# Kernel tuning notes

Hardware: AMD Instinct MI355X
Metric: run time of the kernel (lower is better)

## Reference

```python
import jax, jax.numpy as jnp
import numpy as np

B, H, W, D = 8, 56, 56, 256
NH = 8
KD = D // NH  # 32, key_dim == head_dim (value_factor=1)
FFN = 1024
EPS = 1e-6
SCALE = KD ** -0.5


def _lin(x, w, b):
    # torch nn.Linear: y = x @ W^T + b, W is (out, in)
    return jnp.einsum('...i,oi->...o', x, w) + b


def _ln(x, g, b):
    mu = jnp.mean(x, axis=-1, keepdims=True)
    var = jnp.mean(jnp.square(x - mu), axis=-1, keepdims=True)
    return (x - mu) * jax.lax.rsqrt(var + EPS) * g + b


def _dwconv(x, kernel, bias):
    # x: (B,H,W,C) NHWC, kernel: (kh,kw,1,C) HWIO depthwise
    y = jax.lax.conv_general_dilated(
        x, kernel, window_strides=(1, 1), padding='SAME',
        dimension_numbers=('NHWC', 'HWIO', 'NHWC'),
        feature_group_count=x.shape[-1])
    return y + bias


def _rope_sincos(h, w, head_dim):
    # PosEncodingGen: angle freq repeated pairwise, index over flattened H*W
    angle = 1.0 / (10000.0 ** jnp.linspace(0.0, 1.0, head_dim // 2))
    angle = jnp.repeat(angle, 2)  # (head_dim,)
    idx = jnp.arange(h * w, dtype=jnp.float32)
    phase = idx[:, None] * angle[None, :]
    return jnp.sin(phase).reshape(h, w, head_dim), jnp.cos(phase).reshape(h, w, head_dim)


def _angle_transform(x, sin, cos):
    # x: (B,NH,H,W,KD); sin/cos: (H,W,KD) broadcast over (B,NH)
    x1 = x[..., ::2]
    x2 = x[..., 1::2]
    rot = jnp.stack([-x2, x1], axis=-1).reshape(x.shape)
    return x * cos + rot * sin


def setup_inputs() -> dict:
    key = jax.random.key(0)
    ks = jax.random.split(key, 16)
    s = 0.02
    return {
        'x': jax.random.normal(ks[0], (B, H, W, D), jnp.float32),
        'cpe_w': jax.random.normal(ks[1], (3, 3, 1, D), jnp.float32) * s,
        'cpe_b': jnp.zeros((D,), jnp.float32),
        'ln1_g': jnp.ones((D,), jnp.float32),
        'ln1_b': jnp.zeros((D,), jnp.float32),
        'wq': jax.random.normal(ks[2], (D, D), jnp.float32) * s,
        'bq': jnp.zeros((D,), jnp.float32),
        'wk': jax.random.normal(ks[3], (D, D), jnp.float32) * s,
        'bk': jnp.zeros((D,), jnp.float32),
        'wv': jax.random.normal(ks[4], (D, D), jnp.float32) * s,
        'bv': jnp.zeros((D,), jnp.float32),
        'lepe_w': jax.random.normal(ks[5], (5, 5, 1, D), jnp.float32) * s,
        'lepe_b': jnp.zeros((D,), jnp.float32),
        'wo': jax.random.normal(ks[6], (D, D), jnp.float32) * s,
        'bo': jnp.zeros((D,), jnp.float32),
        'ln2_g': jnp.ones((D,), jnp.float32),
        'ln2_b': jnp.zeros((D,), jnp.float32),
        'fc1_w': jax.random.normal(ks[7], (FFN, D), jnp.float32) * s,
        'fc1_b': jnp.zeros((FFN,), jnp.float32),
        'dw_w': jax.random.normal(ks[8], (3, 3, 1, FFN), jnp.float32) * s,
        'dw_b': jnp.zeros((FFN,), jnp.float32),
        'fc2_w': jax.random.normal(ks[9], (D, FFN), jnp.float32) * s,
        'fc2_b': jnp.zeros((D,), jnp.float32),
    }


def _decomposed_gsa(x, sin, cos, wq, bq, wk, bk, wv, bv, lepe_w, lepe_b, wo, bo):
    b, h, w, d = x.shape
    q = _lin(x, wq, bq)
    k = _lin(x, wk, bk) * SCALE
    v = _lin(x, wv, bv)
    lepe = _dwconv(v, lepe_w, lepe_b)  # (b,h,w,d)
    # -> (b, nh, h, w, kd)
    q = q.reshape(b, h, w, NH, KD).transpose(0, 3, 1, 2, 4)
    k = k.reshape(b, h, w, NH, KD).transpose(0, 3, 1, 2, 4)
    v = v.reshape(b, h, w, NH, KD).transpose(0, 3, 1, 2, 4)
    qr = _angle_transform(q, sin, cos)
    kr = _angle_transform(k, sin, cos)
    # attention along W axis (per row h)
    aw = jnp.einsum('bnhik,bnhjk->bnhij', qr, kr)  # (b,nh,h,w,w)
    aw = jax.nn.softmax(aw, axis=-1)
    vw = jnp.einsum('bnhij,bnhjd->bnhid', aw, v)   # (b,nh,h,w,kd)
    # attention along H axis (per column w)
    ah = jnp.einsum('bniwk,bnjwk->bnwij', qr, kr)  # (b,nh,w,h,h)
    ah = jax.nn.softmax(ah, axis=-1)
    out = jnp.einsum('bnwij,bnjwd->bniwd', ah, vw)  # (b,nh,h,w,kd)
    # faithful to torch: flat reinterpret of (b,nh,h,w,kd) -> (b,h,w,nh*kd)
    out = out.reshape(b, h, w, NH * KD)
    out = out + lepe
    return _lin(out, wo, bo)


def reference(x, cpe_w, cpe_b, ln1_g, ln1_b, wq, bq, wk, bk, wv, bv,
              lepe_w, lepe_b, wo, bo, ln2_g, ln2_b,
              fc1_w, fc1_b, dw_w, dw_b, fc2_w, fc2_b):
    b, h, w, d = x.shape
    x = x + _dwconv(x, cpe_w, cpe_b)
    sin, cos = _rope_sincos(h, w, KD)
    # attention sub-block
    shortcut = x
    xn = _ln(x, ln1_g, ln1_b)
    attn = _decomposed_gsa(xn, sin, cos, wq, bq, wk, bk, wv, bv,
                           lepe_w, lepe_b, wo, bo)
    x = shortcut + attn  # drop_path=Identity, gamma_1=1.0
    # FFN sub-block (subconv=True, subln=False)
    shortcut = x
    xn = _ln(x, ln2_g, ln2_b)
    hdn = jax.nn.gelu(_lin(xn, fc1_w, fc1_b), approximate=False)
    hdn = _dwconv(hdn, dw_w, dw_b) + hdn
    ffn_out = _lin(hdn, fc2_w, fc2_b)
    return shortcut + ffn_out
```

## Files before the change

kernel.cpp:

```cpp
#include <hip/hip_runtime.h>
#include <hip/hip_bf16.h>
#include <math.h>

typedef __hip_bfloat16 bf16;

#define HB 8
#define HH 56
#define WWD 56
#define DD 256
#define NHEAD 8
#define KDIM 32
#define FFND 1024
#define NPIX (HB*HH*WWD)
#define SCALE_K 0.17677669529663687f

typedef __attribute__((ext_vector_type(8))) short short8;
typedef __attribute__((ext_vector_type(4))) float f32x4;

__device__ inline float toF(float x){ return x; }
__device__ inline float toF(bf16 x){ return __bfloat162float(x); }

__device__ inline float bfu_to_f(unsigned short u){
    union { float f; unsigned u32; } cv; cv.u32 = (unsigned)u << 16; return cv.f;
}

__device__ inline unsigned short f2bu(float f){
    union { bf16 b; unsigned short u; } cv; cv.b = __float2bfloat16(f); return cv.u;
}
__device__ inline unsigned pk2(float a, float b){
    return (unsigned)f2bu(a) | ((unsigned)f2bu(b) << 16);
}

__device__ inline void gl16(const bf16* g, unsigned short* l){
    __builtin_amdgcn_global_load_lds((const __attribute__((address_space(1))) void*)g,
                                     (__attribute__((address_space(3))) void*)l, 16, 0, 0);
}

__global__ __launch_bounds__(256) void wcvt_kernel(
    const float* __restrict__ wq, const float* __restrict__ wk,
    const float* __restrict__ wv, const float* __restrict__ wo,
    const float* __restrict__ f1, const float* __restrict__ f2,
    bf16* __restrict__ dst)
{
    const int id = blockIdx.x*256 + threadIdx.x;
    const float* src; int off;
    if      (id < 8192)  { src = wq; off = id; }
    else if (id < 16384) { src = wk; off = id - 8192; }
    else if (id < 24576) { src = wv; off = id - 16384; }
    else if (id < 32768) { src = wo; off = id - 24576; }
    else if (id < 65536) { src = f1; off = id - 32768; }
    else                 { src = f2; off = id - 65536; }
    const float4 a = *(const float4*)(src + (size_t)off*8);
    const float4 b = *(const float4*)(src + (size_t)off*8 + 4);
    uint4 v; v.x = pk2(a.x,a.y); v.y = pk2(a.z,a.w); v.z = pk2(b.x,b.y); v.w = pk2(b.z,b.w);
    *(uint4*)(dst + (size_t)id*8) = v;
}

__global__ __launch_bounds__(256) void rope_init_kernel(float2* __restrict__ t)
{
    const int id = blockIdx.x*256 + threadIdx.x;
    const int idx = id >> 4, i = id & 15;
    const float ph = (float)idx * exp2f(-(float)i * 0.88584749196996324f);
    t[id] = make_float2(cosf(ph), sinf(ph));
}

__global__ __launch_bounds__(256) void cpe_ln_kernel(
    const float* __restrict__ x, const float* __restrict__ wt,
    const float* __restrict__ bias, const float* __restrict__ g,
    const float* __restrict__ bln, float* __restrict__ X0, bf16* __restrict__ B1)
{
    constexpr int C = 256, VEC = 4, CG = 64, PPB = 4, KS = 3, P = 1;
    const int tid = threadIdx.x;
    const int cg  = tid % CG;
    const int pl  = tid / CG;
    const int p   = blockIdx.x * PPB + pl;
    const int w   = p % WWD;
    const int h   = (p / WWD) % HH;
    const int b   = p / (WWD * HH);
    const int c0  = cg * VEC;

    float acc[VEC];
    {
        const float4 b0 = *(const float4*)(bias + c0);
        acc[0] = b0.x; acc[1] = b0.y; acc[2] = b0.z; acc[3] = b0.w;
    }
    #pragma unroll
    for (int ky = 0; ky < KS; ky++) {
        const int hh = h + ky - P;
        if (hh < 0 || hh >= HH) continue;
        #pragma unroll
        for (int kx = 0; kx < KS; kx++) {
            const int ww = w + kx - P;
            if (ww < 0 || ww >= WWD) continue;
            const float4 wv = *(const float4*)(wt + (size_t)(ky*KS + kx)*C + c0);
            const float4 f0 = *(const float4*)(x + ((size_t)((b*HH + hh)*WWD + ww))*C + c0);
            acc[0] += f0.x * wv.x; acc[1] += f0.y * wv.y;
            acc[2] += f0.z * wv.z; acc[3] += f0.w * wv.w;
        }
    }
    const size_t obase = (size_t)p*C + c0;
    {
        const float4 f0 = *(const float4*)(x + obase);
        acc[0] += f0.x; acc[1] += f0.y; acc[2] += f0.z; acc[3] += f0.w;
    }
    { float4 o; o.x = acc[0]; o.y = acc[1]; o.z = acc[2]; o.w = acc[3];
      *(float4*)(X0 + obase) = o; }
    float s1 = acc[0] + acc[1] + acc[2] + acc[3];
    float s2 = acc[0]*acc[0] + acc[1]*acc[1] + acc[2]*acc[2] + acc[3]*acc[3];
    #pragma unroll
    for (int d = 1; d < 64; d <<= 1) { s1 += __shfl_xor(s1, d); s2 += __shfl_xor(s2, d); }
    const float mu  = s1 * (1.0f/DD);
    const float var = s2 * (1.0f/DD) - mu*mu;
    const float inv = rsqrtf(var + 1e-6f);
    const float4 gv = *(const float4*)(g + c0);
    const float4 bv = *(const float4*)(bln + c0);
    uint2 o;
    o.x = pk2((acc[0]-mu)*inv*gv.x + bv.x, (acc[1]-mu)*inv*gv.y + bv.y);
    o.y = pk2((acc[2]-mu)*inv*gv.z + bv.z, (acc[3]-mu)*inv*gv.w + bv.w);
    *(uint2*)(B1 + obase) = o;
}

template<int KS, bool ADD, int C>
__global__ __launch_bounds__(256) void dwconv_slide_kernel(
    const bf16* __restrict__ in, const float* __restrict__ wt, int wst,
    const float* __restrict__ bias, bf16* __restrict__ out)
{
    constexpr int VEC = 8, CG = C/VEC, GPB = 256/CG, NPX = 4, P = KS/2, NX = NPX+KS-1;
    constexpr int GPR = WWD/NPX;
    constexpr int NB  = NPIX/(NPX*GPB);
    const int tid = threadIdx.x;
    const int cg  = tid % CG;
    const int gl  = tid / CG;
    const int bid = blockIdx.x;
    const int swb = (bid & 7) * (NB >> 3) + (bid >> 3);
    const int gid = swb * GPB + gl;
    const int row = gid / GPR;
    const int w0  = (gid % GPR) * NPX;
    const int h   = row % HH;
    const int b   = row / HH;
    const int c0  = cg * VEC;

    float acc[NPX][VEC];
    {
        const float4 b0 = *(const float4*)(bias + c0);
        const float4 b1 = *(const float4*)(bias + c0 + 4);
        #pragma unroll
        for (int j = 0; j < NPX; j++) {
            acc[j][0]=b0.x; acc[j][1]=b0.y; acc[j][2]=b0.z; acc[j][3]=b0.w;
            acc[j][4]=b1.x; acc[j][5]=b1.y; acc[j][6]=b1.z; acc[j][7]=b1.w;
        }
    }

    #pragma unroll
    for (int ky = 0; ky < KS; ky++) {
        const int hh = h + ky - P;
        if (hh < 0 || hh >= HH) continue;
        const bf16* rowp = in + ((size_t)(b*HH + hh) * WWD) * C + c0;
        float wv[KS][VEC];
        #pragma unroll
        for (int kx = 0; kx < KS; kx++) {
            const float* wp = wt + (size_t)(ky*KS + kx)*wst + c0;
            const float4 w0v = *(const float4*)(wp);
            const float4 w1v = *(const float4*)(wp + 4);
            wv[kx][0]=w0v.x; wv[kx][1]=w0v.y; wv[kx][2]=w0v.z; wv[kx][3]=w0v.w;
            wv[kx][4]=w1v.x; wv[kx][5]=w1v.y; wv[kx][6]=w1v.z; wv[kx][7]=w1v.w;
        }
        #pragma unroll
        for (int x = 0; x < NX; x++) {
            const int ww = w0 - P + x;
            short8 raw = {0,0,0,0,0,0,0,0};
            if (ww >= 0 && ww < WWD) raw = *(const short8*)(rowp + (size_t)ww*C);
            float f[VEC];
            #pragma unroll
            for (int e = 0; e < VEC; e++) f[e] = bfu_to_f((unsigned short)raw[e]);
            #pragma unroll
            for (int j = 0; j < NPX; j++) {
                const int kx = x - j;
                if (kx < 0 || kx >= KS) continue;
                #pragma unroll
                for (int e = 0; e < VEC; e++)
                    acc[j][e] += f[e] * wv[kx][e];
            }
        }
    }

    #pragma unroll
    for (int j = 0; j < NPX; j++) {
        const size_t obase = ((size_t)row*WWD + w0 + j)*C + c0;
        if constexpr (ADD) {
            short8 vv = *(const short8*)(in + obase);
            #pragma unroll
            for (int e = 0; e < VEC; e++) acc[j][e] += bfu_to_f((unsigned short)vv[e]);
        }
        uint4 o;
        o.x = pk2(acc[j][0], acc[j][1]); o.y = pk2(acc[j][2], acc[j][3]);
        o.z = pk2(acc[j][4], acc[j][5]); o.w = pk2(acc[j][6], acc[j][7]);
        *(uint4*)(out + obase) = o;
    }
}

__global__ __launch_bounds__(256) void ln_kernel(
    const float* __restrict__ x, const float* __restrict__ g,
    const float* __restrict__ b, bf16* __restrict__ out)
{
    const int wv   = threadIdx.x >> 6;
    const int lane = threadIdx.x & 63;
    const int t    = blockIdx.x * 4 + wv;
    const float4 xv = *(const float4*)(x + (size_t)t*DD + lane*4);
    float s1 = xv.x + xv.y + xv.z + xv.w;
    float s2 = xv.x*xv.x + xv.y*xv.y + xv.z*xv.z + xv.w*xv.w;
    #pragma unroll
    for (int d = 1; d < 64; d <<= 1) {
        s1 += __shfl_xor(s1, d);
        s2 += __shfl_xor(s2, d);
    }
    const float mu  = s1 * (1.0f/DD);
    const float var = s2 * (1.0f/DD) - mu*mu;
    const float inv = rsqrtf(var + 1e-6f);
    const float4 gv = *(const float4*)(g + lane*4);
    const float4 bv = *(const float4*)(b + lane*4);
    uint2 o;
    o.x = pk2((xv.x-mu)*inv*gv.x + bv.x, (xv.y-mu)*inv*gv.y + bv.y);
    o.y = pk2((xv.z-mu)*inv*gv.z + bv.z, (xv.w-mu)*inv*gv.w + bv.w);
    *(uint2*)(out + (size_t)t*DD + lane*4) = o;
}

template<int EPI, int ROPE>
__global__ __launch_bounds__(256) void mgemm128_kernel(
    const bf16* __restrict__ A, const bf16* __restrict__ Wb, int ldw,
    const float* __restrict__ bias, const float2* __restrict__ ropet,
    const float* __restrict__ residF, float* __restrict__ accF,
    bf16* __restrict__ outB, bf16* __restrict__ outK, bf16* __restrict__ outV,
    int M, int N, int K, float scale)
{
    __shared__ __align__(16) unsigned short Sh[16384];
    const int tid  = threadIdx.x;
    const int wid  = tid >> 6;
    const int lane = tid & 63;
    const int quad = lane >> 4;
    const int l15  = lane & 15;
    const int wr   = wid >> 1;
    const int wc   = wid & 1;

    const int NXg = gridDim.x;
    const int T   = NXg * gridDim.y;
    int f = blockIdx.y * NXg + blockIdx.x;
    f = (f & 7) * (T >> 3) + (f >> 3);
    const int row0 = (f / NXg) * 128;
    const int col0 = (f % NXg) * 128;

    f32x4 acc[4][4];
    #pragma unroll
    for (int m = 0; m < 4; m++)
        #pragma unroll
        for (int n = 0; n < 4; n++)
            acc[m][n] = (f32x4){0.f, 0.f, 0.f, 0.f};

    const int ob0 = (wid*2 + 0)*64;
    const int ob1 = (wid*2 + 1)*64;
    const int o0  = ob0 + lane, o1 = ob1 + lane;
    const int rA0 = o0 >> 2, ch0 = (o0 & 3)*8;
    const int rA1 = o1 >> 2, ch1 = (o1 & 3)*8;
    const bf16* pA0 = A  + (size_t)(row0 + rA0)*K   + ch0;
    const bf16* pA1 = A  + (size_t)(row0 + rA1)*K   + ch1;
    const bf16* pW0 = Wb + (size_t)(col0 + rA0)*ldw + ch0;
    const bf16* pW1 = Wb + (size_t)(col0 + rA1)*ldw + ch1;

    #define STAGE(bi) { unsigned short* As_ = Sh + (bi)*8192;                  \
                        unsigned short* Bs_ = Sh + (bi)*8192 + 4096;           \
                        gl16(pA0, &As_[ob0*8]); gl16(pA1, &As_[ob1*8]);        \
                        gl16(pW0, &Bs_[ob0*8]); gl16(pW1, &Bs_[ob1*8]);        \
                        pA0 += 32; pA1 += 32; pW0 += 32; pW1 += 32; }

    #define COMPUTE(bi) { const unsigned short* As_ = Sh + (bi)*8192;          \
                          const unsigned short* Bs_ = Sh + (bi)*8192 + 4096;   \
                          short8 af[4], bfr[4];                                \
                          _Pragma("unroll")                                    \
                          for (int m = 0; m < 4; m++)                          \
                              af[m] = *(const short8*)(&As_[(wr*64 + m*16 + l15)*32 + quad*8]); \
                          _Pragma("unroll")                                    \
                          for (int n = 0; n < 4; n++)                          \
                              bfr[n] = *(const short8*)(&Bs_[(wc*64 + n*16 + l15)*32 + quad*8]); \
                          _Pragma("unroll")                                    \
                          for (int m = 0; m < 4; m++)                          \
                              _Pragma("unroll")                                \
                              for (int n = 0; n < 4; n++)                      \
                                  acc[m][n] = __builtin_amdgcn_mfma_f32_16x16x32_bf16(af[m], bfr[n], acc[m][n], 0, 0, 0); }

    const int nt = K >> 5;
    STAGE(0);
    int cur = 0;
    for (int t = 0; t < nt - 1; t++) {
        STAGE(cur ^ 1);
        asm volatile("s_waitcnt vmcnt(4)" ::: "memory");
        __builtin_amdgcn_s_barrier();
        COMPUTE(cur);
        __builtin_amdgcn_s_barrier();
        cur ^= 1;
    }
    asm volatile("s_waitcnt vmcnt(0)" ::: "memory");
    __builtin_amdgcn_s_barrier();
    COMPUTE(cur);
    #undef STAGE
    #undef COMPUTE

    __syncthreads();
    float* Ls = (float*)Sh;
    const int cbl = l15 * 4;
    const int seg = (EPI == 3) ? (col0 >> 8) : 0;
    bf16* dst = outB;
    if (EPI == 3) dst = (seg == 0) ? outB : ((seg == 1) ? outK : outV);
    const float esc = (EPI == 3) ? ((seg == 1) ? scale : 1.0f) : scale;
    const bool doRope = ROPE && (EPI != 3 || seg < 2);

    #pragma unroll
    for (int m = 0; m < 4; m++) {
        #pragma unroll
        for (int n = 0; n < 4; n++) {
            const int col = n*16 + l15;
            const float bval = bias[col0 + wc*64 + col];
            #pragma unroll
            for (int reg = 0; reg < 4; reg++) {
                float y = (acc[m][n][reg] + bval) * esc;
                if (EPI == 1) y = 0.5f*y*(1.0f + erff(y*0.70710678118654752f));
                Ls[wid*1088 + (quad*4+reg)*68 + col] = y;
            }
        }
        #pragma unroll
        for (int p = 0; p < 4; p++) {
            const int rowt = p*4 + quad;
            const float4 v = *(const float4*)&Ls[wid*1088 + rowt*68 + cbl];
            const int mm = row0 + wr*64 + m*16 + rowt;
            if (EPI == 2) {
                const size_t o = (size_t)mm * N + col0 + wc*64 + cbl;
                const float4 rv = *(const float4*)(residF + o);
                float4 w; w.x = v.x+rv.x; w.y = v.y+rv.y; w.z = v.z+rv.z; w.w = v.w+rv.w;
                *(float4*)(accF + o) = w;
            } else {
                const int ncl = (EPI == 3) ? ((col0 & 255) + wc*64 + cbl)
                                           : (col0 + wc*64 + cbl);
                const size_t o = (EPI == 3) ? ((size_t)mm * 256 + ncl)
                                            : ((size_t)mm * N + ncl);
                float a = v.x, b = v.y, c = v.z, d = v.w;
                if (doRope) {
                    const int idx = mm % (HH*WWD);
                    const int i0 = (ncl & 31) >> 1;
                    const float4 t = *(const float4*)&ropet[(size_t)idx*16 + i0];
                    const float na  = a*t.x - b*t.y;
                    const float nb  = b*t.x + a*t.y;
                    const float ncv = c*t.z - d*t.w;
                    const float nd  = d*t.z + c*t.w;
                    a = na; b = nb; c = ncv; d = nd;
                }
                uint2 ov; ov.x = pk2(a, b); ov.y = pk2(c, d);
                *(uint2*)(dst + o) = ov;
            }
        }
        if (m < 3) __syncthreads();
    }
}

template<bool COLM>
__global__ __launch_bounds__(256) void attn_mfma_kernel(
    const bf16* __restrict__ q, const bf16* __restrict__ k,
    const bf16* __restrict__ v, const bf16* __restrict__ lepe,
    bf16* __restrict__ outp)
{
    __shared__ unsigned short Qb[64*40];
    __shared__ unsigned short Kb[64*40];
    __shared__ unsigned short Vt[32*80];
    __shared__ unsigned short Pb[64*72];

    const int bid  = blockIdx.x;
    const int line = bid % 56;
    const int nh   = (bid / 56) % NHEAD;
    const int b    = bid / (56 * NHEAD);
    const int tid  = threadIdx.x;
    const int wid  = tid >> 6;
    const int lane = tid & 63;
    const int quad = lane >> 4;
    const int l15  = lane & 15;

    const size_t rstr = COLM ? (size_t)WWD * DD : (size_t)DD;
    const size_t base = COLM ? (((size_t)b*HH*WWD + line) * DD + nh*KDIM)
                             : (((size_t)(b*HH + line) * WWD) * DD + nh*KDIM);

    {
        const int r  = tid >> 2;
        const int cc = tid & 3;
        uint4 zero = {0,0,0,0};
        if (r < 56) {
            size_t g = base + (size_t)r * rstr + cc*8;
            *(uint4*)(&Qb[r*40 + cc*8]) = *(const uint4*)(q + g);
            *(uint4*)(&Kb[r*40 + cc*8]) = *(const uint4*)(k + g);
        } else {
            *(uint4*)(&Qb[r*40 + cc*8]) = zero;
            *(uint4*)(&Kb[r*40 + cc*8]) = zero;
        }
        uint4 vv = zero;
        if (lane < 56)
            vv = *(const uint4*)(v + base + (size_t)lane * rstr + wid*8);
        const unsigned short* pv = (const unsigned short*)&vv;
        #pragma unroll
        for (int e = 0; e < 8; e++)
            Vt[(wid*8 + e)*80 + lane] = pv[e];
    }
    __syncthreads();

    {
        short8 af = *(const short8*)(&Qb[(wid*16 + l15)*40 + quad*8]);
        f32x4 s_[4];
        #pragma unroll
        for (int j = 0; j < 4; j++) {
            short8 bfm = *(const short8*)(&Kb[(j*16 + l15)*40 + quad*8]);
            f32x4 z = {0.f,0.f,0.f,0.f};
            s_[j] = __builtin_amdgcn_mfma_f32_16x16x32_bf16(af, bfm, z, 0, 0, 0);
        }
        const bool v3 = (l15 < 8);
        float mx[4], sm[4];
        #pragma unroll
        for (int reg = 0; reg < 4; reg++) {
            float m01 = fmaxf(s_[0][reg], s_[1][reg]);
            float m23 = v3 ? fmaxf(s_[2][reg], s_[3][reg]) : s_[2][reg];
            mx[reg] = fmaxf(m01, m23);
        }
        #pragma unroll
        for (int d = 1; d < 16; d <<= 1) {
            #pragma unroll
            for (int reg = 0; reg < 4; reg++)
                mx[reg] = fmaxf(mx[reg], __shfl_xor(mx[reg], d));
        }
        float e_[4][4];
        #pragma unroll
        for (int reg = 0; reg < 4; reg++) sm[reg] = 0.f;
        #pragma unroll
        for (int j = 0; j < 4; j++) {
            #pragma unroll
            for (int reg = 0; reg < 4; reg++) {
                const bool valid = (j < 3) || v3;
                float ex = valid ? expf(s_[j][reg] - mx[reg]) : 0.f;
                e_[j][reg] = ex;
                sm[reg] += ex;
            }
        }
        #pragma unroll
        for (int d = 1; d < 16; d <<= 1) {
            #pragma unroll
            for (int reg = 0; reg < 4; reg++)
                sm[reg] += __shfl_xor(sm[reg], d);
        }
        float inv[4];
        #pragma unroll
        for (int reg = 0; reg < 4; reg++) inv[reg] = 1.0f / sm[reg];
        #pragma unroll
        for (int j = 0; j < 4; j++)
            #pragma unroll
            for (int reg = 0; reg < 4; reg++)
                Pb[(wid*16 + quad*4 + reg)*72 + j*16 + l15] = f2bu(e_[j][reg] * inv[reg]);
    }
    __syncthreads();

    {
        f32x4 acc[2];
        acc[0] = (f32x4){0.f,0.f,0.f,0.f};
        acc[1] = (f32x4){0.f,0.f,0.f,0.f};
        #pragma unroll
        for (int k0 = 0; k0 < 64; k0 += 32) {
            short8 af = *(const short8*)(&Pb[(wid*16 + l15)*72 + k0 + quad*8]);
            #pragma unroll
            for (int nt = 0; nt < 2; nt++) {
                short8 bfm = *(const short8*)(&Vt[(nt*16 + l15)*80 + k0 + quad*8]);
                acc[nt] = __builtin_amdgcn_mfma_f32_16x16x32_bf16(af, bfm, acc[nt], 0, 0, 0);
            }
        }
        #pragma unroll
        for (int nt = 0; nt < 2; nt++) {
            #pragma unroll
            for (int reg = 0; reg < 4; reg++) {
                const int m = wid*16 + quad*4 + reg;
                const int d = nt*16 + l15;
                if (m < 56) {
                    float val = acc[nt][reg];
                    if (COLM) {
                        int hp = 7*nh + (m >> 3);
                        int wp = (m & 7)*7 + (line >> 3);
                        int cp = (line & 7)*32 + d;
                        size_t o = ((size_t)(b*HH + hp)*WWD + wp)*DD + cp;
                        outp[o] = __float2bfloat16(val + toF(lepe[o]));
                    } else {
                        outp[base + (size_t)m * rstr + d] = __float2bfloat16(val);
                    }
                }
            }
        }
    }
}

extern "C" void kernel_launch(void* const* d_in, const int* in_sizes, int n_in,
                              void* d_out, int out_size, void* d_ws, size_t ws_size,
                              hipStream_t stream)
{
    const float* x_in   = (const float*)d_in[0];
    const float* cpe_w  = (const float*)d_in[1];
    const float* cpe_b  = (const float*)d_in[2];
    const float* ln1_g  = (const float*)d_in[3];
    const float* ln1_b  = (const float*)d_in[4];
    const float* wq     = (const float*)d_in[5];
    const float* bq     = (const float*)d_in[6];
    const float* wk     = (const float*)d_in[7];
    const float* bk     = (const float*)d_in[8];
    const float* wv     = (const float*)d_in[9];
    const float* bv     = (const float*)d_in[10];
    const float* lepe_w = (const float*)d_in[11];
    const float* lepe_b = (const float*)d_in[12];
    const float* wo     = (const float*)d_in[13];
    const float* bo     = (const float*)d_in[14];
    const float* ln2_g  = (const float*)d_in[15];
    const float* ln2_b  = (const float*)d_in[16];
    const float* fc1_w  = (const float*)d_in[17];
    const float* fc1_b  = (const float*)d_in[18];
    const float* dw_w   = (const float*)d_in[19];
    const float* dw_b   = (const float*)d_in[20];
    const float* fc2_w  = (const float*)d_in[21];
    const float* fc2_b  = (const float*)d_in[22];
    float* out = (float*)d_out;

    const size_t ND = (size_t)NPIX * DD;
    const size_t NF = (size_t)NPIX * FFND;
    char* ws = (char*)d_ws;
    float*  X0    = (float*)(ws);
    float*  ACC   = (float*)(ws + ND*4);
    bf16*   B1    = (bf16*) (ws + ND*8);
    bf16*   B2    = (bf16*) (ws + ND*8 + ND*2);
    bf16*   H1    = (bf16*) (ws + ND*8 + ND*4);
    bf16*   H2    = (bf16*) (ws + ND*8 + ND*4 + NF*2);
    bf16*   WB    = (bf16*) (ws + ND*8 + ND*4 + NF*4);
    float2* ROPET = (float2*)(ws + ND*8 + ND*4 + NF*4 + 786432*2);
    float*  BQKV  = (float*) (ws + ND*8 + ND*4 + NF*4 + 786432*2 + 50176*8);
    bf16*   B3 = H1;
    bf16*   B4 = H2;
    bf16*   VWb   = (bf16*)d_out;
    bf16*   ATTNb = VWb + ND;

    const bf16* WOb = WB + 196608;
    const bf16* F1b = WB + 262144;
    const bf16* F2b = WB + 524288;

    dim3 b256(256);
    dim3 gridQKV(768/128, NPIX/128);
    dim3 gridD(DD/128, NPIX/128);
    dim3 gridF(FFND/128, NPIX/128);

    wcvt_kernel<<<384, b256, 0, stream>>>(wq, wk, wv, wo, fc1_w, fc2_w, WB);
    rope_init_kernel<<<196, b256, 0, stream>>>(ROPET);
    hipMemcpyAsync(BQKV,       bq, 256*sizeof(float), hipMemcpyDeviceToDevice, stream);
    hipMemcpyAsync(BQKV + 256, bk, 256*sizeof(float), hipMemcpyDeviceToDevice, stream);
    hipMemcpyAsync(BQKV + 512, bv, 256*sizeof(float), hipMemcpyDeviceToDevice, stream);
    cpe_ln_kernel<<<NPIX/4, b256, 0, stream>>>(x_in, cpe_w, cpe_b, ln1_g, ln1_b, X0, B1);
    mgemm128_kernel<3,1><<<gridQKV, b256, 0, stream>>>(B1, WB, DD, BQKV, ROPET,
                                                       nullptr, nullptr, B2, B3, B4,
                                                       NPIX, 768, DD, SCALE_K);
    dwconv_slide_kernel<5, false, 256><<<784, b256, 0, stream>>>(B4, lepe_w, DD, lepe_b, B1);
    attn_mfma_kernel<false><<<HB*NHEAD*HH, b256, 0, stream>>>(B2, B3, B4, nullptr, VWb);
    attn_mfma_kernel<true><<<HB*NHEAD*WWD, b256, 0, stream>>>(B2, B3, VWb, B1, ATTNb);
    mgemm128_kernel<2,0><<<gridD, b256, 0, stream>>>(ATTNb, WOb, DD, bo, nullptr,
                                                     X0, ACC, nullptr, nullptr, nullptr,
                                                     NPIX, DD, DD, 1.0f);
    ln_kernel<<<NPIX/4, b256, 0, stream>>>(ACC, ln2_g, ln2_b, B2);
    mgemm128_kernel<1,0><<<gridF, b256, 0, stream>>>(B2, F1b, DD, fc1_b, nullptr,
                                                     nullptr, nullptr, H1, nullptr, nullptr,
                                                     NPIX, FFND, DD, 1.0f);
    dwconv_slide_kernel<3, true, 1024><<<3136, b256, 0, stream>>>(H1, dw_w, FFND, dw_b, H2);
    mgemm128_kernel<2,0><<<gridD, b256, 0, stream>>>(H2, F2b, FFND, fc2_b, nullptr,
                                                     ACC, out, nullptr, nullptr, nullptr,
                                                     NPIX, DD, FFND, 1.0f);
}
```

Baseline: 330.5 us.

## Triple-buffer GEMM K-loop and use sliding-window CPE+LayerNorm kernel

The bf16 MFMA GEMM moves from a double-buffered to a triple-buffered LDS pipeline, keeping two K-tiles of global loads in flight and adjusting waitcnt thresholds. The goal is to hide more global-load latency. In exchange, LDS per block grows to 48KB, which lowers occupancy. Separately, the CPE depthwise conv + LayerNorm kernel now has each wave compute 4 adjacent pixels. This reuses loaded input columns and weights across horizontal taps and cuts redundant global reads.

```diff
diff --git a/kernel.cpp b/kernel.cpp
--- a/kernel.cpp
+++ b/kernel.cpp
@@ -64,60 +64,87 @@
     t[id] = make_float2(cosf(ph), sinf(ph));
 }
 
-__global__ __launch_bounds__(256) void cpe_ln_kernel(
+__global__ __launch_bounds__(256) void cpe_ln_slide_kernel(
     const float* __restrict__ x, const float* __restrict__ wt,
     const float* __restrict__ bias, const float* __restrict__ g,
     const float* __restrict__ bln, float* __restrict__ X0, bf16* __restrict__ B1)
 {
-    constexpr int C = 256, VEC = 4, CG = 64, PPB = 4, KS = 3, P = 1;
-    const int tid = threadIdx.x;
-    const int cg  = tid % CG;
-    const int pl  = tid / CG;
-    const int p   = blockIdx.x * PPB + pl;
-    const int w   = p % WWD;
-    const int h   = (p / WWD) % HH;
-    const int b   = p / (WWD * HH);
-    const int c0  = cg * VEC;
-
-    float acc[VEC];
+    constexpr int C = 256, VEC = 4, NPX = 4, KS = 3, P = 1, NX = NPX + KS - 1;
+    constexpr int GPR = WWD / NPX;
+    constexpr int NB  = NPIX / (NPX * 4);
+    const int tid  = threadIdx.x;
+    const int wv   = tid >> 6;
+    const int lane = tid & 63;
+    const int bid  = blockIdx.x;
+    const int swb  = (bid & 7) * (NB >> 3) + (bid >> 3);
+    const int gid  = swb * 4 + wv;
+    const int row  = gid / GPR;
+    const int w0   = (gid % GPR) * NPX;
+    const int h    = row % HH;
+    const int b    = row / HH;
+    const int c0   = lane * VEC;
+
+    float acc[NPX][VEC];
     {
         const float4 b0 = *(const float4*)(bias + c0);
-        acc[0] = b0.x; acc[1] = b0.y; acc[2] = b0.z; acc[3] = b0.w;
-    }
+        #pragma unroll
+        for (int j = 0; j < NPX; j++) {
+            acc[j][0] = b0.x; acc[j][1] = b0.y; acc[j][2] = b0.z; acc[j][3] = b0.w;
+        }
+    }
+
     #pragma unroll
     for (int ky = 0; ky < KS; ky++) {
         const int hh = h + ky - P;
         if (hh < 0 || hh >= HH) continue;
+        const float* rowp = x + ((size_t)(b*HH + hh) * WWD) * C + c0;
+        float wvv[KS][VEC];
         #pragma unroll
         for (int kx = 0; kx < KS; kx++) {
-            const int ww = w + kx - P;
-            if (ww < 0 || ww >= WWD) continue;
-            const float4 wv = *(const float4*)(wt + (size_t)(ky*KS + kx)*C + c0);
-            const float4 f0 = *(const float4*)(x + ((size_t)((b*HH + hh)*WWD + ww))*C + c0);
-            acc[0] += f0.x * wv.x; acc[1] += f0.y * wv.y;
-            acc[2] += f0.z * wv.z; acc[3] += f0.w * wv.w;
-        }
-    }
-    const size_t obase = (size_t)p*C + c0;
-    {
-        const float4 f0 = *(const float4*)(x + obase);
-        acc[0] += f0.x; acc[1] += f0.y; acc[2] += f0.z; acc[3] += f0.w;
-    }
-    { float4 o; o.x = acc[0]; o.y = acc[1]; o.z = acc[2]; o.w = acc[3];
-      *(float4*)(X0 + obase) = o; }
-    float s1 = acc[0] + acc[1] + acc[2] + acc[3];
-    float s2 = acc[0]*acc[0] + acc[1]*acc[1] + acc[2]*acc[2] + acc[3]*acc[3];
-    #pragma unroll
-    for (int d = 1; d < 64; d <<= 1) { s1 += __shfl_xor(s1, d); s2 += __shfl_xor(s2, d); }
-    const float mu  = s1 * (1.0f/DD);
-    const float var = s2 * (1.0f/DD) - mu*mu;
-    const float inv = rsqrtf(var + 1e-6f);
+            const float4 w4 = *(const float4*)(wt + (size_t)(ky*KS + kx)*C + c0);
+            wvv[kx][0] = w4.x; wvv[kx][1] = w4.y; wvv[kx][2] = w4.z; wvv[kx][3] = w4.w;
+        }
+        #pragma unroll
+        for (int xc = 0; xc < NX; xc++) {
+            const int ww = w0 - P + xc;
+            float4 f0 = {0.f, 0.f, 0.f, 0.f};
+            if (ww >= 0 && ww < WWD) f0 = *(const float4*)(rowp + (size_t)ww*C);
+            const float fv[VEC] = {f0.x, f0.y, f0.z, f0.w};
+            #pragma unroll
+            for (int j = 0; j < NPX; j++) {
+                const int kx = xc - j;
+                if (kx < 0 || kx >= KS) continue;
+                #pragma unroll
+                for (int e = 0; e < VEC; e++)
+                    acc[j][e] += fv[e] * wvv[kx][e];
+            }
+        }
+    }
+
     const float4 gv = *(const float4*)(g + c0);
     const float4 bv = *(const float4*)(bln + c0);
-    uint2 o;
-    o.x = pk2((acc[0]-mu)*inv*gv.x + bv.x, (acc[1]-mu)*inv*gv.y + bv.y);
-    o.y = pk2((acc[2]-mu)*inv*gv.z + bv.z, (acc[3]-mu)*inv*gv.w + bv.w);
-    *(uint2*)(B1 + obase) = o;
+    #pragma unroll
+    for (int j = 0; j < NPX; j++) {
+        const size_t obase = ((size_t)row*WWD + w0 + j)*C + c0;
+        {
+            const float4 r0 = *(const float4*)(x + obase);
+            acc[j][0] += r0.x; acc[j][1] += r0.y; acc[j][2] += r0.z; acc[j][3] += r0.w;
+        }
+        { float4 o; o.x = acc[j][0]; o.y = acc[j][1]; o.z = acc[j][2]; o.w = acc[j][3];
+          *(float4*)(X0 + obase) = o; }
+        float s1 = acc[j][0] + acc[j][1] + acc[j][2] + acc[j][3];
+        float s2 = acc[j][0]*acc[j][0] + acc[j][1]*acc[j][1]
+                 + acc[j][2]*acc[j][2] + acc[j][3]*acc[j][3];
+        #pragma unroll
+        for (int d = 1; d < 64; d <<= 1) { s1 += __shfl_xor(s1, d); s2 += __shfl_xor(s2, d); }
+        const float mu  = s1 * (1.0f/DD);
+        const float var = s2 * (1.0f/DD) - mu*mu;
+        const float inv = rsqrtf(var + 1e-6f);
+        uint2 o2;
+        o2.x = pk2((acc[j][0]-mu)*inv*gv.x + bv.x, (acc[j][1]-mu)*inv*gv.y + bv.y);
+        o2.y = pk2((acc[j][2]-mu)*inv*gv.z + bv.z, (acc[j][3]-mu)*inv*gv.w + bv.w);
+        *(uint2*)(B1 + obase) = o2;
+    }
 }
 
 template<int KS, bool ADD, int C>
@@ -233,7 +260,7 @@
     bf16* __restrict__ outB, bf16* __restrict__ outK, bf16* __restrict__ outV,
     int M, int N, int K, float scale)
 {
-    __shared__ __align__(16) unsigned short Sh[16384];
+    __shared__ __align__(16) unsigned short Sh[24576];
     const int tid  = threadIdx.x;
     const int wid  = tid >> 6;
     const int lane = tid & 63;
@@ -267,13 +294,13 @@
     const bf16* pW1 = Wb + (size_t)(col0 + rA1)*ldw + ch1;
 
     #define STAGE(bi) { unsigned short* As_ = Sh + (bi)*8192;                  \
-                        unsigned short* Bs_ = Sh + (bi)*8192 + 4096;           \
+                        unsigned short* Bs_ = As_ + 4096;                      \
                         gl16(pA0, &As_[ob0*8]); gl16(pA1, &As_[ob1*8]);        \
                         gl16(pW0, &Bs_[ob0*8]); gl16(pW1, &Bs_[ob1*8]);        \
                         pA0 += 32; pA1 += 32; pW0 += 32; pW1 += 32; }
 
     #define COMPUTE(bi) { const unsigned short* As_ = Sh + (bi)*8192;          \
-                          const unsigned short* Bs_ = Sh + (bi)*8192 + 4096;   \
+                          const unsigned short* Bs_ = As_ + 4096;              \
                           short8 af[4], bfr[4];                                \
                           _Pragma("unroll")                                    \
                           for (int m = 0; m < 4; m++)                          \
@@ -288,19 +315,23 @@
                                   acc[m][n] = __builtin_amdgcn_mfma_f32_16x16x32_bf16(af[m], bfr[n], acc[m][n], 0, 0, 0); }
 
     const int nt = K >> 5;
-    STAGE(0);
+    STAGE(0); STAGE(1);
     int cur = 0;
-    for (int t = 0; t < nt - 1; t++) {
-        STAGE(cur ^ 1);
-        asm volatile("s_waitcnt vmcnt(4)" ::: "memory");
+    for (int t = 0; t < nt; t++) {
+        if (t + 2 < nt) {
+            const int nx = (cur == 0) ? 2 : ((cur == 1) ? 0 : 1);
+            STAGE(nx);
+            asm volatile("s_waitcnt vmcnt(8)" ::: "memory");
+        } else if (t + 1 < nt) {
+            asm volatile("s_waitcnt vmcnt(4)" ::: "memory");
+        } else {
+            asm volatile("s_waitcnt vmcnt(0)" ::: "memory");
+        }
         __builtin_amdgcn_s_barrier();
         COMPUTE(cur);
-        __builtin_amdgcn_s_barrier();
-        cur ^= 1;
-    }
-    asm volatile("s_waitcnt vmcnt(0)" ::: "memory");
-    __builtin_amdgcn_s_barrier();
-    COMPUTE(cur);
+        if (t + 1 < nt) __builtin_amdgcn_s_barrier();
+        cur = (cur == 2) ? 0 : cur + 1;
+    }
     #undef STAGE
     #undef COMPUTE
 
@@ -556,7 +587,7 @@
     hipMemcpyAsync(BQKV,       bq, 256*sizeof(float), hipMemcpyDeviceToDevice, stream);
     hipMemcpyAsync(BQKV + 256, bk, 256*sizeof(float), hipMemcpyDeviceToDevice, stream);
     hipMemcpyAsync(BQKV + 512, bv, 256*sizeof(float), hipMemcpyDeviceToDevice, stream);
-    cpe_ln_kernel<<<NPIX/4, b256, 0, stream>>>(x_in, cpe_w, cpe_b, ln1_g, ln1_b, X0, B1);
+    cpe_ln_slide_kernel<<<NPIX/16, b256, 0, stream>>>(x_in, cpe_w, cpe_b, ln1_g, ln1_b, X0, B1);
     mgemm128_kernel<3,1><<<gridQKV, b256, 0, stream>>>(B1, WB, DD, BQKV, ROPET,
                                                        nullptr, nullptr, B2, B3, B4,
                                                        NPIX, 768, DD, SCALE_K);
```

Result: no change. 329.7 us (-0.2%).
